# Kernel tuning notes

Hardware: AMD Instinct MI355X
Metric: run time of the kernel (lower is better)

Reference implementation:

```python
import jax, jax.numpy as jnp
import numpy as np

N = 102400   # nodes (256 graphs x 400 nodes)
E = 819200   # edges (avg degree 8)
D = 120      # input_channels
H = 200      # hidden_channels
CC = D + H   # 320 concat dim
L = 400      # nodes per graph (hardcoded view in forward)
B = N // L   # 256 graphs
STEPS = 8
NETYPES = 2


def conv1d(x, w, b):
    # x: [B, C, L], w: [O, I, K] -> [B, O, L-K+1] (VALID, like torch Conv1d)
    y = jax.lax.conv_general_dilated(x, w, (1,), 'VALID',
                                     dimension_numbers=('NCH', 'OIH', 'NCH'))
    return y + b[None, :, None]


def maxpool1d(x, k, s):
    return jax.lax.reduce_window(x, -jnp.inf, jax.lax.max,
                                 (1, 1, k), (1, 1, s), 'VALID')


def setup_inputs():
    key = jax.random.key(0)
    ks = jax.random.split(key, 32)
    g = lambda i, shape, s=0.05: jax.random.normal(ks[i], shape, jnp.float32) * s
    return dict(
        x=g(0, (N, D), 1.0),
        edge_index=jax.random.randint(ks[1], (2, E), 0, N),
        edge_types=jax.random.randint(ks[2], (E,), 0, NETYPES),
        ggnn_W=g(3, (NETYPES, H, H)), ggnn_b=g(4, (NETYPES, H)),
        gru_Wih=g(5, (3 * H, H)), gru_Whh=g(6, (3 * H, H)),
        gru_bih=g(7, (3 * H,)), gru_bhh=g(8, (3 * H,)),
        conv1_w=g(9, (H, H, 3)), conv1_b=g(10, (H,)),
        conv2_w=g(11, (H, H, 1)), conv2_b=g(12, (H,)),
        cconv1_w=g(13, (CC, CC, 3)), cconv1_b=g(14, (CC,)),
        cconv2_w=g(15, (CC, CC, 1)), cconv2_b=g(16, (CC,)),
        mlp_y_w=g(17, (256, H)), mlp_y_b=g(18, (256,)),
        mlp_z_w=g(19, (256, CC)), mlp_z_b=g(20, (256,)),
        ml_l1_w=g(21, (128, 256)), ml_l1_b=g(22, (128,)),
        ml_f1_w=g(23, (64, 128)), ml_f1_b=g(24, (64,)),
        ml_f2_w=g(25, (128, 64)), ml_f2_b=g(26, (128,)),
        cls_w=g(27, (2, 128)), cls_b=g(28, (2,)),
    )


def reference(x, edge_index, edge_types, ggnn_W, ggnn_b, gru_Wih, gru_Whh,
              gru_bih, gru_bhh, conv1_w, conv1_b, conv2_w, conv2_b,
              cconv1_w, cconv1_b, cconv2_w, cconv2_b, mlp_y_w, mlp_y_b,
              mlp_z_w, mlp_z_b, ml_l1_w, ml_l1_b, ml_f1_w, ml_f1_b,
              ml_f2_w, ml_f2_b, cls_w, cls_b):
    src, dst = edge_index[0], edge_index[1]
    emask = [(edge_types == e).astype(x.dtype)[:, None] for e in range(NETYPES)]

    # --- GatedGraphConv: zero-pad feats to H, then 8 steps of
    #     per-etype linear -> gather(src) -> scatter-add(dst) -> GRUCell ---
    h = jnp.pad(x, ((0, 0), (0, H - D)))  # [N, H]
    for _ in range(STEPS):
        a = jnp.zeros((N, H), x.dtype)
        for e in range(NETYPES):
            Wh = h @ ggnn_W[e].T + ggnn_b[e]           # [N, H]
            msg = Wh[src] * emask[e]                    # [E, H]
            a = a + jax.ops.segment_sum(msg, dst, num_segments=N)
        gi = a @ gru_Wih.T + gru_bih                    # [N, 3H]
        gh = h @ gru_Whh.T + gru_bhh                    # [N, 3H]
        ir, iz, inn = jnp.split(gi, 3, axis=-1)
        hr, hz, hn = jnp.split(gh, 3, axis=-1)
        r = jax.nn.sigmoid(ir + hr)
        z = jax.nn.sigmoid(iz + hz)
        n = jnp.tanh(inn + r * hn)
        h = (1.0 - z) * n + z * h
    outputs = h                                         # [N, H]

    # --- conv/pool readout (dropout = identity at eval) ---
    c_i = jnp.concatenate([x, outputs], axis=1).reshape(B, L, CC)
    h_i = outputs.reshape(B, L, H)

    Y1 = maxpool1d(jax.nn.relu(conv1d(h_i.transpose(0, 2, 1), conv1_w, conv1_b)), 3, 2)
    Y2 = maxpool1d(jax.nn.relu(conv1d(Y1, conv2_w, conv2_b)), 2, 2).transpose(0, 2, 1)  # [B,99,H]
    Z1 = maxpool1d(jax.nn.relu(conv1d(c_i.transpose(0, 2, 1), cconv1_w, cconv1_b)), 3, 2)
    Z2 = maxpool1d(jax.nn.relu(conv1d(Z1, cconv2_w, cconv2_b)), 2, 2).transpose(0, 2, 1)  # [B,99,CC]

    before_avg = (Y2 @ mlp_y_w.T + mlp_y_b) * (Z2 @ mlp_z_w.T + mlp_z_b)  # [B,99,256]
    avg = before_avg.mean(axis=1)                                          # [B,256]

    # --- MetricLearningModel head ---
    h1 = jax.nn.relu(avg @ ml_l1_w.T + ml_l1_b)                 # [B,128]
    hf = jax.nn.relu(h1 @ ml_f1_w.T + ml_f1_b)                  # [B,64]
    hf = jax.nn.relu(hf @ ml_f2_w.T + ml_f2_b)                  # [B,128] embedding
    logits = hf @ cls_w.T + cls_b                               # [B,2]
    return logits, hf
```

## Files before the change

### kernel.cpp

```cpp
#include <hip/hip_runtime.h>
#include <hip/hip_bf16.h>
#include <cstdint>
#include <cstddef>

static constexpr int NN = 102400;
static constexpr int EE = 819200;
static constexpr int DD = 120;
static constexpr int HH = 200;
static constexpr int LL = 400;
static constexpr int BB = 256;
static constexpr int NSTEPS = 8;

typedef __attribute__((ext_vector_type(8))) short short8;
typedef __attribute__((ext_vector_type(4))) float f32x4;

__device__ __forceinline__ unsigned short f2bf(float f) {
  union { float f; unsigned u; } v; v.f = f;
  return (unsigned short)((v.u + 0x7fffu + ((v.u >> 16) & 1u)) >> 16);
}
__device__ __forceinline__ float bf2f(unsigned short s) {
  union { unsigned u; float f; } v; v.u = ((unsigned)s) << 16; return v.f;
}

template<int AMODE, int ASRC, int OBF, int RELU, int EPI>
__global__ __launch_bounds__(256) void gemm_mfma(
    const void* __restrict__ Asrc, const void* __restrict__ A2,
    const short* __restrict__ WP, const float* __restrict__ bias,
    void* __restrict__ Cdst, int M, int Nout, int K, int KT,
    const float* __restrict__ tt0, const float* __restrict__ tt1,
    const float* __restrict__ cnt2, float* __restrict__ hout,
    unsigned short* __restrict__ hbout)
{
  __shared__ short Asm[4096];
  __shared__ short Bsm[4096];
  const int tid = threadIdx.x;
  const int row0 = blockIdx.y * 128;
  const int col0 = blockIdx.x * 128;

  f32x4 acc[4][4];
#pragma unroll
  for (int mi = 0; mi < 4; mi++)
#pragma unroll
    for (int ni = 0; ni < 4; ni++) acc[mi][ni] = (f32x4){0.f, 0.f, 0.f, 0.f};

  const int r = tid & 15;
  const int kgl = (tid >> 4) & 3;
  const int ghalf = tid >> 6;
  const int w = tid >> 6, l = tid & 63;
  const int wr = w >> 1, wc = w & 1;

  for (int t = 0; t < KT; t++) {
#pragma unroll
    for (int half = 0; half < 2; half++) {
      const int g = ghalf + half * 4;
      int row = row0 + g * 16 + r;
      if (row >= M) row = M - 1;
      const int k0 = t * 32 + kgl * 8;
      short8 sv;
      bool direct = false;
      if (AMODE == 0 && ASRC == 1) {
        if (k0 < K) {
          sv = *reinterpret_cast<const short8*>(
              (const unsigned short*)Asrc + (size_t)row * K + k0);
          direct = true;
        }
      } else if (AMODE == 1) {
        if (k0 < K) {
          const int b = row / 398, tt = row - b * 398;
          const int tap = k0 / 200, i0 = k0 - tap * 200;
          sv = *reinterpret_cast<const short8*>(
              (const unsigned short*)Asrc + ((size_t)(b * 400 + tt + tap)) * 200 + i0);
          direct = true;
        }
      } else if (AMODE == 3) {
        if (k0 < 400) {
          sv = *reinterpret_cast<const short8*>(
              (const unsigned short*)Asrc + (size_t)row * 400 + k0);
          direct = true;
        } else if (k0 < 600) {
          sv = *reinterpret_cast<const short8*>(
              (const unsigned short*)A2 + (size_t)row * 200 + (k0 - 400));
          direct = true;
        }
      } else if (AMODE == 2) {
        if (k0 < K) {
          const int b = row / 398, tt = row - b * 398;
          const int tap = k0 / 320, c0 = k0 - tap * 320;
          const int node = b * 400 + tt + tap;
          if (c0 < 120) {
            const float* p = (const float*)A2 + (size_t)node * 120 + c0;
            const float4 x0 = *reinterpret_cast<const float4*>(p);
            const float4 x1 = *reinterpret_cast<const float4*>(p + 4);
            sv[0] = (short)f2bf(x0.x); sv[1] = (short)f2bf(x0.y);
            sv[2] = (short)f2bf(x0.z); sv[3] = (short)f2bf(x0.w);
            sv[4] = (short)f2bf(x1.x); sv[5] = (short)f2bf(x1.y);
            sv[6] = (short)f2bf(x1.z); sv[7] = (short)f2bf(x1.w);
            direct = true;
          } else {
            sv = *reinterpret_cast<const short8*>(
                (const unsigned short*)Asrc + (size_t)node * 200 + (c0 - 120));
            direct = true;
          }
        }
      } else {
        if (k0 < K) {
          const float* p = (const float*)Asrc + (size_t)row * K + k0;
          const float4 x0 = *reinterpret_cast<const float4*>(p);
          const float4 x1 = *reinterpret_cast<const float4*>(p + 4);
          sv[0] = (short)f2bf(x0.x); sv[1] = (short)f2bf(x0.y);
          sv[2] = (short)f2bf(x0.z); sv[3] = (short)f2bf(x0.w);
          sv[4] = (short)f2bf(x1.x); sv[5] = (short)f2bf(x1.y);
          sv[6] = (short)f2bf(x1.z); sv[7] = (short)f2bf(x1.w);
          direct = true;
        }
      }
      if (!direct) {
#pragma unroll
        for (int j = 0; j < 8; j++) sv[j] = 0;
      }
      *reinterpret_cast<short8*>(&Asm[(g * 64 + (tid & 63)) * 8]) = sv;
    }
    {
      const size_t wbase = ((size_t)blockIdx.x * KT + t) * 4096;
#pragma unroll
      for (int it = 0; it < 2; it++) {
        const int idx = it * 256 + tid;
        *reinterpret_cast<short8*>(&Bsm[idx * 8]) =
            *reinterpret_cast<const short8*>(WP + wbase + (size_t)idx * 8);
      }
    }
    __syncthreads();
    short8 af[4], bfr[4];
#pragma unroll
    for (int mi = 0; mi < 4; mi++)
      af[mi] = *reinterpret_cast<const short8*>(&Asm[((wr * 4 + mi) * 64 + l) * 8]);
#pragma unroll
    for (int ni = 0; ni < 4; ni++)
      bfr[ni] = *reinterpret_cast<const short8*>(&Bsm[((wc * 4 + ni) * 64 + l) * 8]);
#pragma unroll
    for (int mi = 0; mi < 4; mi++)
#pragma unroll
      for (int ni = 0; ni < 4; ni++)
        acc[mi][ni] = __builtin_amdgcn_mfma_f32_16x16x32_bf16(
            af[mi], bfr[ni], acc[mi][ni], 0, 0, 0);
    __syncthreads();
  }

  if (EPI == 0) {
#pragma unroll
    for (int mi = 0; mi < 4; mi++)
#pragma unroll
      for (int ni = 0; ni < 4; ni++) {
        const int col = col0 + wc * 64 + ni * 16 + (l & 15);
        if (col < Nout) {
          const float bbv = bias ? bias[col] : 0.f;
          const int rbase = row0 + wr * 64 + mi * 16 + ((l >> 4) << 2);
#pragma unroll
          for (int q = 0; q < 4; q++) {
            const int row = rbase + q;
            if (row < M) {
              float val = acc[mi][ni][q] + bbv;
              if (RELU) val = fmaxf(val, 0.f);
              if (OBF)
                ((unsigned short*)Cdst)[(size_t)row * Nout + col] = f2bf(val);
              else
                ((float*)Cdst)[(size_t)row * Nout + col] = val;
            }
          }
        }
      }
  } else {
    const int g = l & 3;
#pragma unroll
    for (int mi = 0; mi < 4; mi++) {
#pragma unroll
      for (int q = 0; q < 4; q++) {
        const int row = row0 + wr * 64 + mi * 16 + ((l >> 4) << 2) + q;
        const float2 cc = *reinterpret_cast<const float2*>(cnt2 + (size_t)row * 2);
#pragma unroll
        for (int ni = 0; ni < 4; ni++) {
          const int col = col0 + wc * 64 + ni * 16 + (l & 15);
          float val = acc[mi][ni][q] + bias[col] + cc.x * tt0[col] + cc.y * tt1[col];
          float av;
          if (g == 0 || g == 1) av = 1.f / (1.f + expf(-val));
          else av = val;
          const float x1 = __shfl_xor(av, 1);
          const float x2 = __shfl_xor(av, 2);
          const float x3 = __shfl_xor(av, 3);
          if (g == 2 && col < 800) {
            const int ch = col >> 2;
            const float nv = tanhf(av + x2 * x1);
            float hold;
            if (hout) hold = hout[(size_t)row * 200 + ch];
            else hold = bf2f(((const unsigned short*)A2)[(size_t)row * 200 + ch]);
            const float hnew = (1.f - x3) * nv + x3 * hold;
            if (hout) hout[(size_t)row * 200 + ch] = hnew;
            hbout[(size_t)row * 200 + ch] = f2bf(hnew);
          }
        }
      }
    }
  }
}

__global__ void pack_w(const float* __restrict__ W, short* __restrict__ WP,
                       int Nout, int K, int Ntp, int Kp, int CIN) {
  const int KT = Kp >> 5;
  const int total = (Ntp >> 7) * KT * 512;
  const int u = blockIdx.x * 256 + threadIdx.x;
  if (u >= total) return;
  const int l = u & 63;
  const int g = (u >> 6) & 7;
  const int T = (u >> 9) % KT;
  const int ct = (u >> 9) / KT;
  const int n = ct * 128 + g * 16 + (l & 15);
  const int kb = T * 32 + ((l >> 4) << 3);
  short8 sv;
#pragma unroll
  for (int j = 0; j < 8; j++) {
    const int k = kb + j;
    float v = 0.f;
    if (n < Nout && k < K) {
      if (CIN > 0) {
        const int kw = k / CIN, i = k - kw * CIN;
        v = W[((size_t)n * CIN + i) * 3 + kw];
      } else {
        v = W[(size_t)n * K + k];
      }
    }
    sv[j] = (short)f2bf(v);
  }
  *reinterpret_cast<short8*>(&WP[(size_t)u * 8]) = sv;
}

__global__ void fill_kernel(float* __restrict__ p, int n, float v) {
  const int t = blockIdx.x * 256 + threadIdx.x;
  if (t < n) p[t] = v;
}

__global__ void pad_h_kernel(const float* __restrict__ x, float* __restrict__ h,
                             unsigned short* __restrict__ hb) {
  const int t = blockIdx.x * 256 + threadIdx.x;
  if (t >= NN * HH) return;
  const int n = t / HH, j = t - n * HH;
  const float v = (j < DD) ? x[(size_t)n * DD + j] : 0.0f;
  if (h) h[t] = v;
  hb[t] = f2bf(v);
}

__global__ void hist_kernel(const int* __restrict__ ei, int* __restrict__ cnt) {
  const int e = blockIdx.x * 256 + threadIdx.x;
  if (e < EE) atomicAdd(&cnt[ei[EE + e]], 1);
}
__global__ void scan1_kernel(const int* __restrict__ cnt, int* __restrict__ ex,
                             int* __restrict__ bsum) {
  __shared__ int sm[256];
  const int tid = threadIdx.x;
  const int i = blockIdx.x * 256 + tid;
  const int v = cnt[i];
  sm[tid] = v; __syncthreads();
  for (int off = 1; off < 256; off <<= 1) {
    int t = (tid >= off) ? sm[tid - off] : 0;
    __syncthreads();
    sm[tid] += t;
    __syncthreads();
  }
  ex[i] = sm[tid] - v;
  if (tid == 255) bsum[blockIdx.x] = sm[255];
}
__global__ void scan2_kernel(int* __restrict__ bsum, int nb) {
  if (threadIdx.x == 0 && blockIdx.x == 0) {
    int run = 0;
    for (int b = 0; b < nb; b++) { int t = bsum[b]; bsum[b] = run; run += t; }
  }
}
__global__ void scan3_kernel(const int* __restrict__ ex, const int* __restrict__ bsum,
                             int* __restrict__ rowptr) {
  const int i = blockIdx.x * 256 + threadIdx.x;
  if (i < NN) rowptr[i] = ex[i] + bsum[i >> 8];
  if (i == 0) rowptr[NN] = EE;
}
__global__ void fillcsr_kernel(const int* __restrict__ ei, const int* __restrict__ et,
                               const int* __restrict__ rowptr, int* __restrict__ fcur,
                               int* __restrict__ eidx) {
  const int e = blockIdx.x * 256 + threadIdx.x;
  if (e >= EE) return;
  const int d = ei[EE + e];
  const int pos = atomicAdd(&fcur[d], 1);
  eidx[rowptr[d] + pos] = (ei[e] << 1) | (et[e] & 1);
}
__global__ void count_kernel(const int* __restrict__ ei, const int* __restrict__ et,
                             float* __restrict__ cnt2) {
  const int e = blockIdx.x * 256 + threadIdx.x;
  if (e >= EE) return;
  atomicAdd(&cnt2[(size_t)ei[EE + e] * 2 + (et[e] & 1)], 1.0f);
}

__global__ void wcat2_kernel(const float* __restrict__ gw, float* __restrict__ W2) {
  const int t = blockIdx.x * 256 + threadIdx.x;
  if (t >= 400 * 200) return;
  const int m = t / 200, j = t - m * 200;
  const int ty = (m < 200) ? 0 : 1;
  const int kk = m - ty * 200;
  W2[t] = gw[(size_t)ty * 40000 + j * 200 + kk];
}
__global__ void ta_kernel(const float* __restrict__ wih, const float* __restrict__ gb,
                          float* __restrict__ ta) {
  const int o = blockIdx.x * 256 + threadIdx.x;
  if (o >= 1200) return;
  const int which = o / 600, oo = o - which * 600;
  float s = 0.f;
  for (int j = 0; j < 200; j++) s += wih[(size_t)oo * 200 + j] * gb[which * 200 + j];
  ta[o] = s;
}
__global__ void wfd_kernel(const float* __restrict__ M1, const float* __restrict__ whh,
                           float* __restrict__ WFD) {
  const int t = blockIdx.x * 256 + threadIdx.x;
  if (t >= 800 * 600) return;
  const int c = t / 600, k = t - c * 600;
  const int ch = c >> 2, g = c & 3;
  float v = 0.f;
  if (g == 0) v = (k < 400) ? M1[(size_t)ch * 400 + k] : whh[(size_t)ch * 200 + (k - 400)];
  else if (g == 1) v = (k < 400) ? M1[(size_t)(200 + ch) * 400 + k]
                                 : whh[(size_t)(200 + ch) * 200 + (k - 400)];
  else if (g == 2) v = (k < 400) ? M1[(size_t)(400 + ch) * 400 + k] : 0.f;
  else v = (k < 400) ? 0.f : whh[(size_t)(400 + ch) * 200 + (k - 400)];
  WFD[t] = v;
}
__global__ void bbtt_kernel(const float* __restrict__ bih, const float* __restrict__ bhh,
                            const float* __restrict__ ta, float* __restrict__ bb,
                            float* __restrict__ tt0, float* __restrict__ tt1) {
  const int c = blockIdx.x * 256 + threadIdx.x;
  if (c >= 896) return;
  const int ch = c >> 2, g = c & 3;
  float b = 0.f, t0 = 0.f, t1 = 0.f;
  if (ch < 200) {
    if (g == 0) b = bih[ch] + bhh[ch];
    else if (g == 1) b = bih[200 + ch] + bhh[200 + ch];
    else if (g == 2) b = bih[400 + ch];
    else b = bhh[400 + ch];
    if (g < 3) { t0 = ta[g * 200 + ch]; t1 = ta[600 + g * 200 + ch]; }
  }
  bb[c] = b; tt0[c] = t0; tt1[c] = t1;
}

__global__ void gather_kernel(const unsigned short* __restrict__ hb,
                              const int* __restrict__ rowptr,
                              const int* __restrict__ eidx,
                              unsigned short* __restrict__ s) {
  const int nid = blockIdx.x * 4 + (threadIdx.x >> 6);
  const int l = threadIdx.x & 63;
  if (nid >= NN) return;
  const int beg = rowptr[nid], end = rowptr[nid + 1];
  float a00 = 0, a01 = 0, a10 = 0, a11 = 0;
  float b00 = 0, b01 = 0, b10 = 0, b11 = 0;
  const unsigned int* H32 = (const unsigned int*)hb;
  for (int e = beg; e < end; e++) {
    const int pe = eidx[e];
    const int src = pe >> 1, ty = pe & 1;
    const unsigned int* hr = H32 + (size_t)src * 100;
    const unsigned int u0 = hr[l];
    unsigned int u1 = 0;
    if (l < 36) u1 = hr[64 + l];
    const float f0 = bf2f((unsigned short)(u0 & 0xffffu));
    const float f1 = bf2f((unsigned short)(u0 >> 16));
    const float f2 = bf2f((unsigned short)(u1 & 0xffffu));
    const float f3 = bf2f((unsigned short)(u1 >> 16));
    if (ty == 0) { a00 += f0; a01 += f1; a10 += f2; a11 += f3; }
    else         { b00 += f0; b01 += f1; b10 += f2; b11 += f3; }
  }
  unsigned int* S32 = (unsigned int*)s;
  const size_t rb = (size_t)nid * 200;
  S32[rb + l] = (unsigned int)f2bf(a00) | ((unsigned int)f2bf(a01) << 16);
  S32[rb + 100 + l] = (unsigned int)f2bf(b00) | ((unsigned int)f2bf(b01) << 16);
  if (l < 36) {
    S32[rb + 64 + l] = (unsigned int)f2bf(a10) | ((unsigned int)f2bf(a11) << 16);
    S32[rb + 164 + l] = (unsigned int)f2bf(b10) | ((unsigned int)f2bf(b11) << 16);
  }
}

__global__ void pool_kernel(const float* __restrict__ src, float* __restrict__ dst,
                            int nb, int Lin, int Lout, int C, int win) {
  const size_t t = (size_t)blockIdx.x * 256 + threadIdx.x;
  const size_t tot = (size_t)nb * Lout * C;
  if (t >= tot) return;
  const int c = (int)(t % C);
  const size_t bp = t / C;
  const int p = (int)(bp % Lout);
  const int b = (int)(bp / Lout);
  const float* s0 = src + ((size_t)b * Lin + 2 * p) * C + c;
  float v = s0[0];
  for (int q = 1; q < win; q++) v = fmaxf(v, s0[(size_t)q * C]);
  dst[t] = v;
}

__global__ void prodmean_kernel(const float* __restrict__ y, const float* __restrict__ z,
                                float* __restrict__ avg, int g0, int nb) {
  const int t = blockIdx.x * 256 + threadIdx.x;
  if (t >= nb * 256) return;
  const int b = t >> 8, j = t & 255;
  const float* yr = y + (size_t)b * 99 * 256 + j;
  const float* zr = z + (size_t)b * 99 * 256 + j;
  float sum = 0.0f;
  for (int p = 0; p < 99; p++) sum += yr[(size_t)p * 256] * zr[(size_t)p * 256];
  avg[(size_t)(g0 + b) * 256 + j] = sum * (1.0f / 99.0f);
}

extern "C" void kernel_launch(void* const* d_in, const int* in_sizes, int n_in,
                              void* d_out, int out_size, void* d_ws, size_t ws_size,
                              hipStream_t stream) {
  const float* x       = (const float*)d_in[0];
  const int*   ei      = (const int*)d_in[1];
  const int*   et      = (const int*)d_in[2];
  const float* ggnn_W  = (const float*)d_in[3];
  const float* ggnn_b  = (const float*)d_in[4];
  const float* gru_Wih = (const float*)d_in[5];
  const float* gru_Whh = (const float*)d_in[6];
  const float* gru_bih = (const float*)d_in[7];
  const float* gru_bhh = (const float*)d_in[8];
  const float* conv1_w = (const float*)d_in[9];
  const float* conv1_b = (const float*)d_in[10];
  const float* conv2_w = (const float*)d_in[11];
  const float* conv2_b = (const float*)d_in[12];
  const float* cconv1_w = (const float*)d_in[13];
  const float* cconv1_b = (const float*)d_in[14];
  const float* cconv2_w = (const float*)d_in[15];
  const float* cconv2_b = (const float*)d_in[16];
  const float* mlp_y_w = (const float*)d_in[17];
  const float* mlp_y_b = (const float*)d_in[18];
  const float* mlp_z_w = (const float*)d_in[19];
  const float* mlp_z_b = (const float*)d_in[20];
  const float* ml_l1_w = (const float*)d_in[21];
  const float* ml_l1_b = (const float*)d_in[22];
  const float* ml_f1_w = (const float*)d_in[23];
  const float* ml_f1_b = (const float*)d_in[24];
  const float* ml_f2_w = (const float*)d_in[25];
  const float* ml_f2_b = (const float*)d_in[26];
  const float* cls_w   = (const float*)d_in[27];
  const float* cls_b   = (const float*)d_in[28];
  float* out = (float*)d_out;

  char* base = (char*)d_ws;
  size_t off = 0;
  auto alloc = [&](size_t bytes) { char* p = base + off; off += (bytes + 15) & ~(size_t)15; return p; };
  unsigned short* s   = (unsigned short*)alloc(81920000);
  unsigned short* hb1 = (unsigned short*)alloc(40960000);
  unsigned short* hb0 = (unsigned short*)alloc(40960000);
  int* eidx    = (int*)alloc(3276800);
  int* rowptr  = (int*)alloc(409604);
  float* cnt2  = (float*)alloc(819200);
  short* WPF   = (short*)alloc(1089536);
  short* WPwc  = (short*)alloc(229376);
  short* WPc1  = (short*)alloc(311296);
  short* WPcc1 = (short*)alloc(737280);
  short* WPc2  = (short*)alloc(114688);
  short* WPcc2 = (short*)alloc(245760);
  short* WPmy  = (short*)alloc(114688);
  short* WPmz  = (short*)alloc(163840);
  short* WPl1  = (short*)alloc(65536);
  short* WPf1  = (short*)alloc(32768);
  short* WPf2  = (short*)alloc(16384);
  short* WPcls = (short*)alloc(32768);
  float* bb  = (float*)alloc(3584);
  float* tt0 = (float*)alloc(3584);
  float* tt1 = (float*)alloc(3584);
  float* avg = (float*)alloc(262144);
  float* h1b = (float*)alloc(131072);
  float* hf1 = (float*)alloc(65536);
  const size_t persist = off;
  float* h = (float*)alloc(81920000);
  const bool has_h = (ws_size >= off);

  const int fill_blocks = (out_size + 255) / 256;
  if (ws_size < persist) {
    fill_kernel<<<fill_blocks, 256, 0, stream>>>(out, out_size,
                                                 -(float)(ws_size >> 20));
    return;
  }
  float* hptr = has_h ? h : nullptr;

  char* ali = (char*)s;
  float* Wcat2 = (float*)(ali);
  float* M1f   = (float*)(ali + 320000);
  float* WFD   = (float*)(ali + 1280000);
  float* ta    = (float*)(ali + 3200000);
  int* cnt     = (int*)(ali + 3204800);
  int* ex      = (int*)(ali + 3614400);
  int* bsum    = (int*)(ali + 4024000);
  int* fcur    = (int*)(ali + 4025600);

  fill_kernel<<<fill_blocks, 256, 0, stream>>>(out, out_size, 1.0e4f);

  pad_h_kernel<<<80000, 256, 0, stream>>>(x, hptr, hb0);
  hipMemsetAsync(cnt, 0, 409600, stream);
  hipMemsetAsync(fcur, 0, 409600, stream);
  hipMemsetAsync(cnt2, 0, 819200, stream);
  hist_kernel<<<3200, 256, 0, stream>>>(ei, cnt);
  scan1_kernel<<<400, 256, 0, stream>>>(cnt, ex, bsum);
  scan2_kernel<<<1, 64, 0, stream>>>(bsum, 400);
  scan3_kernel<<<400, 256, 0, stream>>>(ex, bsum, rowptr);
  fillcsr_kernel<<<3200, 256, 0, stream>>>(ei, et, rowptr, fcur, eidx);
  count_kernel<<<3200, 256, 0, stream>>>(ei, et, cnt2);

  auto packs = [&](const float* W, short* WP, int Nout, int K, int Ntp, int Kp, int CIN) {
    const int total = (Ntp >> 7) * (Kp >> 5) * 512;
    pack_w<<<(total + 255) / 256, 256, 0, stream>>>(W, WP, Nout, K, Ntp, Kp, CIN);
  };
  wcat2_kernel<<<313, 256, 0, stream>>>(ggnn_W, Wcat2);
  packs(Wcat2, WPwc, 400, 200, 512, 224, 0);
  gemm_mfma<0, 0, 0, 0, 0><<<dim3(4, 5), 256, 0, stream>>>(
      gru_Wih, nullptr, WPwc, nullptr, M1f, 600, 400, 200, 7,
      nullptr, nullptr, nullptr, nullptr, nullptr);
  ta_kernel<<<5, 256, 0, stream>>>(gru_Wih, ggnn_b, ta);
  wfd_kernel<<<1875, 256, 0, stream>>>(M1f, gru_Whh, WFD);
  packs(WFD, WPF, 800, 600, 896, 608, 0);
  bbtt_kernel<<<4, 256, 0, stream>>>(gru_bih, gru_bhh, ta, bb, tt0, tt1);
  packs(conv1_w, WPc1,  200, 600, 256, 608, 200);
  packs(cconv1_w,WPcc1, 320, 960, 384, 960, 320);
  packs(conv2_w, WPc2,  200, 200, 256, 224, 0);
  packs(cconv2_w,WPcc2, 320, 320, 384, 320, 0);
  packs(mlp_y_w, WPmy,  256, 200, 256, 224, 0);
  packs(mlp_z_w, WPmz,  256, 320, 256, 320, 0);
  packs(ml_l1_w, WPl1,  128, 256, 128, 256, 0);
  packs(ml_f1_w, WPf1,   64, 128, 128, 128, 0);
  packs(ml_f2_w, WPf2,  128,  64, 128,  64, 0);
  packs(cls_w,   WPcls,   2, 128, 128, 128, 0);

  unsigned short* hbb[2] = {hb0, hb1};
  for (int step = 0; step < NSTEPS; step++) {
    unsigned short* hcur = hbb[step & 1];
    unsigned short* hnxt = hbb[(step & 1) ^ 1];
    gather_kernel<<<25600, 256, 0, stream>>>(hcur, rowptr, eidx, s);
    gemm_mfma<3, 1, 0, 0, 2><<<dim3(7, 800), 256, 0, stream>>>(
        s, hcur, WPF, bb, nullptr, NN, 896, 600, 19,
        tt0, tt1, cnt2, hptr, hnxt);
  }

  const int G = 64;
  float* b0  = (float*)s;
  float* b1  = b0 + (size_t)G * 127360;
  float* b2  = b1 + (size_t)G * 63360;
  float* y2c = b2 + (size_t)G * 63360;
  float* z2c = y2c + (size_t)G * 19800;

  for (int g0 = 0; g0 < BB; g0 += G) {
    const unsigned short* hc = hb0 + (size_t)g0 * LL * HH;
    const float* xc = x + (size_t)g0 * LL * DD;
    const int M1 = G * 398, M2 = G * 198, M3 = G * 99;
    const int gy1 = (M1 + 127) / 128, gy2 = (M2 + 127) / 128, gy3 = (M3 + 127) / 128;
    gemm_mfma<1, 1, 0, 1, 0><<<dim3(2, gy1), 256, 0, stream>>>(
        hc, nullptr, WPc1, conv1_b, b0, M1, 200, 600, 19,
        nullptr, nullptr, nullptr, nullptr, nullptr);
    pool_kernel<<<(int)(((size_t)G * 198 * 200 + 255) / 256), 256, 0, stream>>>(
        b0, b1, G, 398, 198, 200, 3);
    gemm_mfma<0, 0, 0, 1, 0><<<dim3(2, gy2), 256, 0, stream>>>(
        b1, nullptr, WPc2, conv2_b, b2, M2, 200, 200, 7,
        nullptr, nullptr, nullptr, nullptr, nullptr);
    pool_kernel<<<(int)(((size_t)G * 99 * 200 + 255) / 256), 256, 0, stream>>>(
        b2, y2c, G, 198, 99, 200, 2);
    gemm_mfma<2, 1, 0, 1, 0><<<dim3(3, gy1), 256, 0, stream>>>(
        hc, xc, WPcc1, cconv1_b, b0, M1, 320, 960, 30,
        nullptr, nullptr, nullptr, nullptr, nullptr);
    pool_kernel<<<(int)(((size_t)G * 198 * 320 + 255) / 256), 256, 0, stream>>>(
        b0, b1, G, 398, 198, 320, 3);
    gemm_mfma<0, 0, 0, 1, 0><<<dim3(3, gy2), 256, 0, stream>>>(
        b1, nullptr, WPcc2, cconv2_b, b2, M2, 320, 320, 10,
        nullptr, nullptr, nullptr, nullptr, nullptr);
    pool_kernel<<<(int)(((size_t)G * 99 * 320 + 255) / 256), 256, 0, stream>>>(
        b2, z2c, G, 198, 99, 320, 2);
    gemm_mfma<0, 0, 0, 0, 0><<<dim3(2, gy3), 256, 0, stream>>>(
        y2c, nullptr, WPmy, mlp_y_b, b0, M3, 256, 200, 7,
        nullptr, nullptr, nullptr, nullptr, nullptr);
    gemm_mfma<0, 0, 0, 0, 0><<<dim3(2, gy3), 256, 0, stream>>>(
        z2c, nullptr, WPmz, mlp_z_b, b1, M3, 256, 320, 10,
        nullptr, nullptr, nullptr, nullptr, nullptr);
    prodmean_kernel<<<(G * 256 + 255) / 256, 256, 0, stream>>>(b0, b1, avg, g0, G);
  }

  gemm_mfma<0, 0, 0, 1, 0><<<dim3(1, 2), 256, 0, stream>>>(
      avg, nullptr, WPl1, ml_l1_b, h1b, 256, 128, 256, 8,
      nullptr, nullptr, nullptr, nullptr, nullptr);
  gemm_mfma<0, 0, 0, 1, 0><<<dim3(1, 2), 256, 0, stream>>>(
      h1b, nullptr, WPf1, ml_f1_b, hf1, 256, 64, 128, 4,
      nullptr, nullptr, nullptr, nullptr, nullptr);
  gemm_mfma<0, 0, 0, 1, 0><<<dim3(1, 2), 256, 0, stream>>>(
      hf1, nullptr, WPf2, ml_f2_b, out + 512, 256, 128, 64, 2,
      nullptr, nullptr, nullptr, nullptr, nullptr);
  gemm_mfma<0, 0, 0, 0, 0><<<dim3(1, 2), 256, 0, stream>>>(
      out + 512, nullptr, WPcls, cls_b, out, 256, 2, 128, 4,
      nullptr, nullptr, nullptr, nullptr, nullptr);
}
```

Baseline: 5.957 ms.

## Add dedicated GGNN step kernel keeping A rows resident in LDS across column tiles

Replaces the generic GEMM with GRU epilogue for each GGNN step with a dedicated kernel. Each block stages a 64-row slice of the concatenated [aggregated messages | h] input (K=600) in shared memory once, then loops over all 7 column tiles, streaming packed weights straight from global memory into registers with one-step prefetch. This removes the repeated A reloads across the 7 column-tile blocks of the old grid, at the cost of about 76KB of LDS per block, which limits occupancy, and of B fragments read from global/L2 without LDS sharing.

Result: slower. 9.480 ms (+59.1%).

```diff
diff --git a/kernel.cpp b/kernel.cpp
--- a/kernel.cpp
+++ b/kernel.cpp
@@ -70,16 +70,6 @@
           const int tap = k0 / 200, i0 = k0 - tap * 200;
           sv = *reinterpret_cast<const short8*>(
               (const unsigned short*)Asrc + ((size_t)(b * 400 + tt + tap)) * 200 + i0);
-          direct = true;
-        }
-      } else if (AMODE == 3) {
-        if (k0 < 400) {
-          sv = *reinterpret_cast<const short8*>(
-              (const unsigned short*)Asrc + (size_t)row * 400 + k0);
-          direct = true;
-        } else if (k0 < 600) {
-          sv = *reinterpret_cast<const short8*>(
-              (const unsigned short*)A2 + (size_t)row * 200 + (k0 - 400));
           direct = true;
         }
       } else if (AMODE == 2) {
@@ -146,53 +136,117 @@
     __syncthreads();
   }
 
-  if (EPI == 0) {
-#pragma unroll
-    for (int mi = 0; mi < 4; mi++)
-#pragma unroll
-      for (int ni = 0; ni < 4; ni++) {
-        const int col = col0 + wc * 64 + ni * 16 + (l & 15);
-        if (col < Nout) {
-          const float bbv = bias ? bias[col] : 0.f;
-          const int rbase = row0 + wr * 64 + mi * 16 + ((l >> 4) << 2);
-#pragma unroll
-          for (int q = 0; q < 4; q++) {
-            const int row = rbase + q;
-            if (row < M) {
-              float val = acc[mi][ni][q] + bbv;
-              if (RELU) val = fmaxf(val, 0.f);
-              if (OBF)
-                ((unsigned short*)Cdst)[(size_t)row * Nout + col] = f2bf(val);
-              else
-                ((float*)Cdst)[(size_t)row * Nout + col] = val;
-            }
+#pragma unroll
+  for (int mi = 0; mi < 4; mi++)
+#pragma unroll
+    for (int ni = 0; ni < 4; ni++) {
+      const int col = col0 + wc * 64 + ni * 16 + (l & 15);
+      if (col < Nout) {
+        const float bbv = bias ? bias[col] : 0.f;
+        const int rbase = row0 + wr * 64 + mi * 16 + ((l >> 4) << 2);
+#pragma unroll
+        for (int q = 0; q < 4; q++) {
+          const int row = rbase + q;
+          if (row < M) {
+            float val = acc[mi][ni][q] + bbv;
+            if (RELU) val = fmaxf(val, 0.f);
+            if (OBF)
+              ((unsigned short*)Cdst)[(size_t)row * Nout + col] = f2bf(val);
+            else
+              ((float*)Cdst)[(size_t)row * Nout + col] = val;
           }
         }
       }
-  } else {
-    const int g = l & 3;
+    }
+}
+
+__global__ __launch_bounds__(256) void ggnn_step_kernel(
+    const unsigned short* __restrict__ s,
+    const unsigned short* __restrict__ hb,
+    const short* __restrict__ WPF,
+    const float* __restrict__ bbv,
+    const float* __restrict__ tt0, const float* __restrict__ tt1,
+    const float* __restrict__ cnt2,
+    float* __restrict__ hout,
+    unsigned short* __restrict__ hbout)
+{
+  __shared__ short Asm[38912];
+  const int tid = threadIdx.x;
+  const int row0 = blockIdx.x * 64;
+  const int l = tid & 63;
+  const int w = tid >> 6;
+
+  {
+    const int rr = l & 15;
+    const int kg = l >> 4;
+    const int row = row0 + w * 16 + rr;
+    const unsigned short* srow = s + (size_t)row * 400;
+    const unsigned short* hrow = hb + (size_t)row * 200;
+#pragma unroll
+    for (int kt = 0; kt < 19; ++kt) {
+      const int k0 = kt * 32 + kg * 8;
+      short8 sv;
+      if (k0 < 400) {
+        sv = *reinterpret_cast<const short8*>(srow + k0);
+      } else if (k0 < 600) {
+        sv = *reinterpret_cast<const short8*>(hrow + (k0 - 400));
+      } else {
+#pragma unroll
+        for (int j = 0; j < 8; j++) sv[j] = 0;
+      }
+      *reinterpret_cast<short8*>(&Asm[kt * 2048 + tid * 8]) = sv;
+    }
+  }
+  __syncthreads();
+
+  for (int ct = 0; ct < 7; ++ct) {
+    f32x4 acc[4][2];
 #pragma unroll
     for (int mi = 0; mi < 4; mi++) {
-#pragma unroll
-      for (int q = 0; q < 4; q++) {
-        const int row = row0 + wr * 64 + mi * 16 + ((l >> 4) << 2) + q;
+      acc[mi][0] = (f32x4){0.f, 0.f, 0.f, 0.f};
+      acc[mi][1] = (f32x4){0.f, 0.f, 0.f, 0.f};
+    }
+    const short* Bbase = WPF + (((size_t)ct * 19 * 8) + (size_t)w * 2) * 512 + (size_t)l * 8;
+    short8 b0 = *reinterpret_cast<const short8*>(Bbase);
+    short8 b1 = *reinterpret_cast<const short8*>(Bbase + 512);
+    for (int kt = 0; kt < 19; ++kt) {
+      const int ktn = (kt < 18) ? kt + 1 : 18;
+      const short8 n0 = *reinterpret_cast<const short8*>(Bbase + (size_t)ktn * 4096);
+      const short8 n1 = *reinterpret_cast<const short8*>(Bbase + (size_t)ktn * 4096 + 512);
+      short8 af[4];
+#pragma unroll
+      for (int mi = 0; mi < 4; mi++)
+        af[mi] = *reinterpret_cast<const short8*>(&Asm[kt * 2048 + (mi * 64 + l) * 8]);
+#pragma unroll
+      for (int mi = 0; mi < 4; mi++) {
+        acc[mi][0] = __builtin_amdgcn_mfma_f32_16x16x32_bf16(af[mi], b0, acc[mi][0], 0, 0, 0);
+        acc[mi][1] = __builtin_amdgcn_mfma_f32_16x16x32_bf16(af[mi], b1, acc[mi][1], 0, 0, 0);
+      }
+      b0 = n0; b1 = n1;
+    }
+    const int gq = l & 3;
+#pragma unroll
+    for (int mi = 0; mi < 4; ++mi) {
+#pragma unroll
+      for (int q = 0; q < 4; ++q) {
+        const int row = row0 + mi * 16 + ((l >> 4) << 2) + q;
         const float2 cc = *reinterpret_cast<const float2*>(cnt2 + (size_t)row * 2);
 #pragma unroll
-        for (int ni = 0; ni < 4; ni++) {
-          const int col = col0 + wc * 64 + ni * 16 + (l & 15);
-          float val = acc[mi][ni][q] + bias[col] + cc.x * tt0[col] + cc.y * tt1[col];
+        for (int ni = 0; ni < 2; ++ni) {
+          const int col = ct * 128 + w * 32 + ni * 16 + (l & 15);
+          float val = acc[mi][ni][q] + bbv[col] + cc.x * tt0[col] + cc.y * tt1[col];
           float av;
-          if (g == 0 || g == 1) av = 1.f / (1.f + expf(-val));
+          if (gq == 0 || gq == 1) av = 1.f / (1.f + expf(-val));
           else av = val;
           const float x1 = __shfl_xor(av, 1);
           const float x2 = __shfl_xor(av, 2);
           const float x3 = __shfl_xor(av, 3);
-          if (g == 2 && col < 800) {
+          if (gq == 2 && col < 800) {
             const int ch = col >> 2;
             const float nv = tanhf(av + x2 * x1);
             float hold;
             if (hout) hold = hout[(size_t)row * 200 + ch];
-            else hold = bf2f(((const unsigned short*)A2)[(size_t)row * 200 + ch]);
+            else hold = bf2f(hb[(size_t)row * 200 + ch]);
             const float hnew = (1.f - x3) * nv + x3 * hold;
             if (hout) hout[(size_t)row * 200 + ch] = hnew;
             hbout[(size_t)row * 200 + ch] = f2bf(hnew);
@@ -531,9 +585,8 @@
     unsigned short* hcur = hbb[step & 1];
     unsigned short* hnxt = hbb[(step & 1) ^ 1];
     gather_kernel<<<25600, 256, 0, stream>>>(hcur, rowptr, eidx, s);
-    gemm_mfma<3, 1, 0, 0, 2><<<dim3(7, 800), 256, 0, stream>>>(
-        s, hcur, WPF, bb, nullptr, NN, 896, 600, 19,
-        tt0, tt1, cnt2, hptr, hnxt);
+    ggnn_step_kernel<<<1600, 256, 0, stream>>>(
+        s, hcur, WPF, bb, tt0, tt1, cnt2, hptr, hnxt);
   }
 
   const int G = 64;
```

## Add dedicated GGNN GEMM with direct-to-LDS loads and padded concatenated A buffer

Applied to the files above, without the earlier changes.

The gather kernel now writes a single padded [N,608] bf16 row holding both edge-type aggregates plus a copy of the current hidden state. This lets a new dedicated GGNN GEMM kernel stream A and packed weights straight into shared memory with global_load_lds, with no per-element address branching or register staging. Workgroup IDs are remapped across 8 groups, apparently to spread consecutive tiles across XCDs for cache locality. The cost is extra gather writes and a larger scratch buffer.

After: 6.429 ms. 1.08x slower.

```diff
diff --git a/kernel.cpp b/kernel.cpp
--- a/kernel.cpp
+++ b/kernel.cpp
@@ -22,14 +22,17 @@
   union { unsigned u; float f; } v; v.u = ((unsigned)s) << 16; return v.f;
 }
 
-template<int AMODE, int ASRC, int OBF, int RELU, int EPI>
+__device__ __forceinline__ void gload_lds16(const void* g, void* lds) {
+  __builtin_amdgcn_global_load_lds(
+      (const __attribute__((address_space(1))) void*)g,
+      (__attribute__((address_space(3))) void*)lds, 16, 0, 0);
+}
+
+template<int AMODE, int ASRC, int OBF, int RELU>
 __global__ __launch_bounds__(256) void gemm_mfma(
     const void* __restrict__ Asrc, const void* __restrict__ A2,
     const short* __restrict__ WP, const float* __restrict__ bias,
-    void* __restrict__ Cdst, int M, int Nout, int K, int KT,
-    const float* __restrict__ tt0, const float* __restrict__ tt1,
-    const float* __restrict__ cnt2, float* __restrict__ hout,
-    unsigned short* __restrict__ hbout)
+    void* __restrict__ Cdst, int M, int Nout, int K, int KT)
 {
   __shared__ short Asm[4096];
   __shared__ short Bsm[4096];
@@ -70,16 +73,6 @@
           const int tap = k0 / 200, i0 = k0 - tap * 200;
           sv = *reinterpret_cast<const short8*>(
               (const unsigned short*)Asrc + ((size_t)(b * 400 + tt + tap)) * 200 + i0);
-          direct = true;
-        }
-      } else if (AMODE == 3) {
-        if (k0 < 400) {
-          sv = *reinterpret_cast<const short8*>(
-              (const unsigned short*)Asrc + (size_t)row * 400 + k0);
-          direct = true;
-        } else if (k0 < 600) {
-          sv = *reinterpret_cast<const short8*>(
-              (const unsigned short*)A2 + (size_t)row * 200 + (k0 - 400));
           direct = true;
         }
       } else if (AMODE == 2) {
@@ -146,57 +139,113 @@
     __syncthreads();
   }
 
-  if (EPI == 0) {
-#pragma unroll
-    for (int mi = 0; mi < 4; mi++)
-#pragma unroll
-      for (int ni = 0; ni < 4; ni++) {
-        const int col = col0 + wc * 64 + ni * 16 + (l & 15);
-        if (col < Nout) {
-          const float bbv = bias ? bias[col] : 0.f;
-          const int rbase = row0 + wr * 64 + mi * 16 + ((l >> 4) << 2);
-#pragma unroll
-          for (int q = 0; q < 4; q++) {
-            const int row = rbase + q;
-            if (row < M) {
-              float val = acc[mi][ni][q] + bbv;
-              if (RELU) val = fmaxf(val, 0.f);
-              if (OBF)
-                ((unsigned short*)Cdst)[(size_t)row * Nout + col] = f2bf(val);
-              else
-                ((float*)Cdst)[(size_t)row * Nout + col] = val;
-            }
+#pragma unroll
+  for (int mi = 0; mi < 4; mi++)
+#pragma unroll
+    for (int ni = 0; ni < 4; ni++) {
+      const int col = col0 + wc * 64 + ni * 16 + (l & 15);
+      if (col < Nout) {
+        const float bbv = bias ? bias[col] : 0.f;
+        const int rbase = row0 + wr * 64 + mi * 16 + ((l >> 4) << 2);
+#pragma unroll
+        for (int q = 0; q < 4; q++) {
+          const int row = rbase + q;
+          if (row < M) {
+            float val = acc[mi][ni][q] + bbv;
+            if (RELU) val = fmaxf(val, 0.f);
+            if (OBF)
+              ((unsigned short*)Cdst)[(size_t)row * Nout + col] = f2bf(val);
+            else
+              ((float*)Cdst)[(size_t)row * Nout + col] = val;
           }
         }
       }
-  } else {
-    const int g = l & 3;
-#pragma unroll
-    for (int mi = 0; mi < 4; mi++) {
-#pragma unroll
-      for (int q = 0; q < 4; q++) {
-        const int row = row0 + wr * 64 + mi * 16 + ((l >> 4) << 2) + q;
-        const float2 cc = *reinterpret_cast<const float2*>(cnt2 + (size_t)row * 2);
-#pragma unroll
-        for (int ni = 0; ni < 4; ni++) {
-          const int col = col0 + wc * 64 + ni * 16 + (l & 15);
-          float val = acc[mi][ni][q] + bias[col] + cc.x * tt0[col] + cc.y * tt1[col];
-          float av;
-          if (g == 0 || g == 1) av = 1.f / (1.f + expf(-val));
-          else av = val;
-          const float x1 = __shfl_xor(av, 1);
-          const float x2 = __shfl_xor(av, 2);
-          const float x3 = __shfl_xor(av, 3);
-          if (g == 2 && col < 800) {
-            const int ch = col >> 2;
-            const float nv = tanhf(av + x2 * x1);
-            float hold;
-            if (hout) hold = hout[(size_t)row * 200 + ch];
-            else hold = bf2f(((const unsigned short*)A2)[(size_t)row * 200 + ch]);
-            const float hnew = (1.f - x3) * nv + x3 * hold;
-            if (hout) hout[(size_t)row * 200 + ch] = hnew;
-            hbout[(size_t)row * 200 + ch] = f2bf(hnew);
-          }
+    }
+}
+
+__global__ __launch_bounds__(256) void ggnn_gemm_kernel(
+    const unsigned short* __restrict__ s2,
+    const short* __restrict__ WPF,
+    const float* __restrict__ bbv,
+    const float* __restrict__ tt0, const float* __restrict__ tt1,
+    const float* __restrict__ cnt2,
+    const unsigned short* __restrict__ hbold,
+    float* __restrict__ hout,
+    unsigned short* __restrict__ hbout)
+{
+  __shared__ short Asm[4096];
+  __shared__ short Bsm[4096];
+  const int tid = threadIdx.x;
+  const int w = tid >> 6, l = tid & 63;
+  const int wr = w >> 1, wc = w & 1;
+  const int hwid = blockIdx.y * 7 + blockIdx.x;
+  const int wgid = (hwid & 7) * 700 + (hwid >> 3);
+  const int rowt = wgid / 7;
+  const int ct = wgid - rowt * 7;
+  const int row0 = rowt * 128;
+
+  f32x4 acc[4][4];
+#pragma unroll
+  for (int mi = 0; mi < 4; mi++)
+#pragma unroll
+    for (int ni = 0; ni < 4; ni++) acc[mi][ni] = (f32x4){0.f, 0.f, 0.f, 0.f};
+
+  const int arow = (l & 15);
+  const int akol = (l >> 4) * 8;
+
+  for (int t = 0; t < 19; t++) {
+#pragma unroll
+    for (int gi = 0; gi < 2; gi++) {
+      const int g = w + gi * 4;
+      const unsigned short* ap =
+          s2 + (size_t)(row0 + g * 16 + arow) * 608 + t * 32 + akol;
+      gload_lds16(ap, &Asm[g * 512]);
+      const short* bp = WPF + ((((size_t)ct * 19 + t) * 8 + g) * 64 + l) * 8;
+      gload_lds16(bp, &Bsm[g * 512]);
+    }
+    __syncthreads();
+    short8 af[4], bfr[4];
+#pragma unroll
+    for (int mi = 0; mi < 4; mi++)
+      af[mi] = *reinterpret_cast<const short8*>(&Asm[((wr * 4 + mi) * 64 + l) * 8]);
+#pragma unroll
+    for (int ni = 0; ni < 4; ni++)
+      bfr[ni] = *reinterpret_cast<const short8*>(&Bsm[((wc * 4 + ni) * 64 + l) * 8]);
+#pragma unroll
+    for (int mi = 0; mi < 4; mi++)
+#pragma unroll
+      for (int ni = 0; ni < 4; ni++)
+        acc[mi][ni] = __builtin_amdgcn_mfma_f32_16x16x32_bf16(
+            af[mi], bfr[ni], acc[mi][ni], 0, 0, 0);
+    __syncthreads();
+  }
+
+  const int gq = l & 3;
+#pragma unroll
+  for (int mi = 0; mi < 4; mi++) {
+#pragma unroll
+    for (int q = 0; q < 4; q++) {
+      const int row = row0 + wr * 64 + mi * 16 + ((l >> 4) << 2) + q;
+      const float2 cc = *reinterpret_cast<const float2*>(cnt2 + (size_t)row * 2);
+#pragma unroll
+      for (int ni = 0; ni < 4; ni++) {
+        const int col = ct * 128 + wc * 64 + ni * 16 + (l & 15);
+        float val = acc[mi][ni][q] + bbv[col] + cc.x * tt0[col] + cc.y * tt1[col];
+        float av;
+        if (gq == 0 || gq == 1) av = 1.f / (1.f + expf(-val));
+        else av = val;
+        const float x1 = __shfl_xor(av, 1);
+        const float x2 = __shfl_xor(av, 2);
+        const float x3 = __shfl_xor(av, 3);
+        if (gq == 2 && col < 800) {
+          const int ch = col >> 2;
+          const float nv = tanhf(av + x2 * x1);
+          float hold;
+          if (hout) hold = hout[(size_t)row * 200 + ch];
+          else hold = bf2f(hbold[(size_t)row * 200 + ch]);
+          const float hnew = (1.f - x3) * nv + x3 * hold;
+          if (hout) hout[(size_t)row * 200 + ch] = hnew;
+          hbout[(size_t)row * 200 + ch] = f2bf(hnew);
         }
       }
     }
@@ -347,7 +396,7 @@
 __global__ void gather_kernel(const unsigned short* __restrict__ hb,
                               const int* __restrict__ rowptr,
                               const int* __restrict__ eidx,
-                              unsigned short* __restrict__ s) {
+                              unsigned short* __restrict__ s2) {
   const int nid = blockIdx.x * 4 + (threadIdx.x >> 6);
   const int l = threadIdx.x & 63;
   if (nid >= NN) return;
@@ -369,14 +418,18 @@
     if (ty == 0) { a00 += f0; a01 += f1; a10 += f2; a11 += f3; }
     else         { b00 += f0; b01 += f1; b10 += f2; b11 += f3; }
   }
-  unsigned int* S32 = (unsigned int*)s;
-  const size_t rb = (size_t)nid * 200;
+  unsigned int* S32 = (unsigned int*)s2;
+  const size_t rb = (size_t)nid * 304;
+  const unsigned int* hn = H32 + (size_t)nid * 100;
   S32[rb + l] = (unsigned int)f2bf(a00) | ((unsigned int)f2bf(a01) << 16);
   S32[rb + 100 + l] = (unsigned int)f2bf(b00) | ((unsigned int)f2bf(b01) << 16);
+  S32[rb + 200 + l] = hn[l];
   if (l < 36) {
     S32[rb + 64 + l] = (unsigned int)f2bf(a10) | ((unsigned int)f2bf(a11) << 16);
     S32[rb + 164 + l] = (unsigned int)f2bf(b10) | ((unsigned int)f2bf(b11) << 16);
-  }
+    S32[rb + 264 + l] = hn[64 + l];
+  }
+  if (l < 4) S32[rb + 300 + l] = 0;
 }
 
 __global__ void pool_kernel(const float* __restrict__ src, float* __restrict__ dst,
@@ -443,7 +496,7 @@
   char* base = (char*)d_ws;
   size_t off = 0;
   auto alloc = [&](size_t bytes) { char* p = base + off; off += (bytes + 15) & ~(size_t)15; return p; };
-  unsigned short* s   = (unsigned short*)alloc(81920000);
+  unsigned short* s2  = (unsigned short*)alloc(124518400);
   unsigned short* hb1 = (unsigned short*)alloc(40960000);
   unsigned short* hb0 = (unsigned short*)alloc(40960000);
   int* eidx    = (int*)alloc(3276800);
@@ -479,7 +532,7 @@
   }
   float* hptr = has_h ? h : nullptr;
 
-  char* ali = (char*)s;
+  char* ali = (char*)s2;
   float* Wcat2 = (float*)(ali);
   float* M1f   = (float*)(ali + 320000);
   float* WFD   = (float*)(ali + 1280000);
@@ -508,9 +561,8 @@
   };
   wcat2_kernel<<<313, 256, 0, stream>>>(ggnn_W, Wcat2);
   packs(Wcat2, WPwc, 400, 200, 512, 224, 0);
-  gemm_mfma<0, 0, 0, 0, 0><<<dim3(4, 5), 256, 0, stream>>>(
-      gru_Wih, nullptr, WPwc, nullptr, M1f, 600, 400, 200, 7,
-      nullptr, nullptr, nullptr, nullptr, nullptr);
+  gemm_mfma<0, 0, 0, 0><<<dim3(4, 5), 256, 0, stream>>>(
+      gru_Wih, nullptr, WPwc, nullptr, M1f, 600, 400, 200, 7);
   ta_kernel<<<5, 256, 0, stream>>>(gru_Wih, ggnn_b, ta);
   wfd_kernel<<<1875, 256, 0, stream>>>(M1f, gru_Whh, WFD);
   packs(WFD, WPF, 800, 600, 896, 608, 0);
@@ -530,14 +582,13 @@
   for (int step = 0; step < NSTEPS; step++) {
     unsigned short* hcur = hbb[step & 1];
     unsigned short* hnxt = hbb[(step & 1) ^ 1];
-    gather_kernel<<<25600, 256, 0, stream>>>(hcur, rowptr, eidx, s);
-    gemm_mfma<3, 1, 0, 0, 2><<<dim3(7, 800), 256, 0, stream>>>(
-        s, hcur, WPF, bb, nullptr, NN, 896, 600, 19,
-        tt0, tt1, cnt2, hptr, hnxt);
+    gather_kernel<<<25600, 256, 0, stream>>>(hcur, rowptr, eidx, s2);
+    ggnn_gemm_kernel<<<dim3(7, 800), 256, 0, stream>>>(
+        s2, WPF, bb, tt0, tt1, cnt2, hcur, hptr, hnxt);
   }
 
   const int G = 64;
-  float* b0  = (float*)s;
+  float* b0  = (float*)s2;
   float* b1  = b0 + (size_t)G * 127360;
   float* b2  = b1 + (size_t)G * 63360;
   float* y2c = b2 + (size_t)G * 63360;
@@ -548,45 +599,35 @@
     const float* xc = x + (size_t)g0 * LL * DD;
     const int M1 = G * 398, M2 = G * 198, M3 = G * 99;
     const int gy1 = (M1 + 127) / 128, gy2 = (M2 + 127) / 128, gy3 = (M3 + 127) / 128;
-    gemm_mfma<1, 1, 0, 1, 0><<<dim3(2, gy1), 256, 0, stream>>>(
-        hc, nullptr, WPc1, conv1_b, b0, M1, 200, 600, 19,
-        nullptr, nullptr, nullptr, nullptr, nullptr);
+    gemm_mfma<1, 1, 0, 1><<<dim3(2, gy1), 256, 0, stream>>>(
+        hc, nullptr, WPc1, conv1_b, b0, M1, 200, 600, 19);
     pool_kernel<<<(int)(((size_t)G * 198 * 200 + 255) / 256), 256, 0, stream>>>(
         b0, b1, G, 398, 198, 200, 3);
-    gemm_mfma<0, 0, 0, 1, 0><<<dim3(2, gy2), 256, 0, stream>>>(
-        b1, nullptr, WPc2, conv2_b, b2, M2, 200, 200, 7,
-        nullptr, nullptr, nullptr, nullptr, nullptr);
+    gemm_mfma<0, 0, 0, 1><<<dim3(2, gy2), 256, 0, stream>>>(
+        b1, nullptr, WPc2, conv2_b, b2, M2, 200, 200, 7);
     pool_kernel<<<(int)(((size_t)G * 99 * 200 + 255) / 256), 256, 0, stream>>>(
         b2, y2c, G, 198, 99, 200, 2);
-    gemm_mfma<2, 1, 0, 1, 0><<<dim3(3, gy1), 256, 0, stream>>>(
-        hc, xc, WPcc1, cconv1_b, b0, M1, 320, 960, 30,
-        nullptr, nullptr, nullptr, nullptr, nullptr);
+    gemm_mfma<2, 1, 0, 1><<<dim3(3, gy1), 256, 0, stream>>>(
+        hc, xc, WPcc1, cconv1_b, b0, M1, 320, 960, 30);
     pool_kernel<<<(int)(((size_t)G * 198 * 320 + 255) / 256), 256, 0, stream>>>(
         b0, b1, G, 398, 198, 320, 3);
-    gemm_mfma<0, 0, 0, 1, 0><<<dim3(3, gy2), 256, 0, stream>>>(
-        b1, nullptr, WPcc2, cconv2_b, b2, M2, 320, 320, 10,
-        nullptr, nullptr, nullptr, nullptr, nullptr);
+    gemm_mfma<0, 0, 0, 1><<<dim3(3, gy2), 256, 0, stream>>>(
+        b1, nullptr, WPcc2, cconv2_b, b2, M2, 320, 320, 10);
     pool_kernel<<<(int)(((size_t)G * 99 * 320 + 255) / 256), 256, 0, stream>>>(
         b2, z2c, G, 198, 99, 320, 2);
-    gemm_mfma<0, 0, 0, 0, 0><<<dim3(2, gy3), 256, 0, stream>>>(
-        y2c, nullptr, WPmy, mlp_y_b, b0, M3, 256, 200, 7,
-        nullptr, nullptr, nullptr, nullptr, nullptr);
-    gemm_mfma<0, 0, 0, 0, 0><<<dim3(2, gy3), 256, 0, stream>>>(
-        z2c, nullptr, WPmz, mlp_z_b, b1, M3, 256, 320, 10,
-        nullptr, nullptr, nullptr, nullptr, nullptr);
+    gemm_mfma<0, 0, 0, 0><<<dim3(2, gy3), 256, 0, stream>>>(
+        y2c, nullptr, WPmy, mlp_y_b, b0, M3, 256, 200, 7);
+    gemm_mfma<0, 0, 0, 0><<<dim3(2, gy3), 256, 0, stream>>>(
+        z2c, nullptr, WPmz, mlp_z_b, b1, M3, 256, 320, 10);
     prodmean_kernel<<<(G * 256 + 255) / 256, 256, 0, stream>>>(b0, b1, avg, g0, G);
   }
 
-  gemm_mfma<0, 0, 0, 1, 0><<<dim3(1, 2), 256, 0, stream>>>(
-      avg, nullptr, WPl1, ml_l1_b, h1b, 256, 128, 256, 8,
-      nullptr, nullptr, nullptr, nullptr, nullptr);
-  gemm_mfma<0, 0, 0, 1, 0><<<dim3(1, 2), 256, 0, stream>>>(
-      h1b, nullptr, WPf1, ml_f1_b, hf1, 256, 64, 128, 4,
-      nullptr, nullptr, nullptr, nullptr, nullptr);
-  gemm_mfma<0, 0, 0, 1, 0><<<dim3(1, 2), 256, 0, stream>>>(
-      hf1, nullptr, WPf2, ml_f2_b, out + 512, 256, 128, 64, 2,
-      nullptr, nullptr, nullptr, nullptr, nullptr);
-  gemm_mfma<0, 0, 0, 0, 0><<<dim3(1, 2), 256, 0, stream>>>(
-      out + 512, nullptr, WPcls, cls_b, out, 256, 2, 128, 4,
-      nullptr, nullptr, nullptr, nullptr, nullptr);
-}
+  gemm_mfma<0, 0, 0, 1><<<dim3(1, 2), 256, 0, stream>>>(
+      avg, nullptr, WPl1, ml_l1_b, h1b, 256, 128, 256, 8);
+  gemm_mfma<0, 0, 0, 1><<<dim3(1, 2), 256, 0, stream>>>(
+      h1b, nullptr, WPf1, ml_f1_b, hf1, 256, 64, 128, 4);
+  gemm_mfma<0, 0, 0, 1><<<dim3(1, 2), 256, 0, stream>>>(
+      hf1, nullptr, WPf2, ml_f2_b, out + 512, 256, 128, 64, 2);
+  gemm_mfma<0, 0, 0, 0><<<dim3(1, 2), 256, 0, stream>>>(
+      out + 512, nullptr, WPcls, cls_b, out, 256, 2, 128, 4);
+}
```
